# Kernel tuning notes

Measured on AMD Instinct MI355X. Metric: run time of the kernel, lower is better.

Reference implementation:

```python
import jax, jax.numpy as jnp
import numpy as np

N_NODES = 40000
N_EDGES = 640000
D_IN = 512
D_OUT = 128


def setup_inputs() -> dict:
    key = jax.random.key(0)
    k_x, k_w, k_a, k_v, k_r, k_c = jax.random.split(key, 6)
    # Xavier-uniform bound for Linear(in=512, out=128)
    bound = float(np.sqrt(6.0 / (D_IN + D_OUT)))
    x = jax.random.normal(k_x, (N_NODES, D_IN), dtype=jnp.float32)
    weight = jax.random.uniform(k_w, (D_OUT, D_IN), dtype=jnp.float32,
                                minval=-bound, maxval=bound)
    bias = jnp.zeros((D_OUT,), dtype=jnp.float32)
    # PReLU default init is 0.25 (single shared slope)
    alpha = jnp.full((1,), 0.25, dtype=jnp.float32)
    edge_val = jax.random.uniform(k_v, (N_EDGES,), dtype=jnp.float32)
    edge_row = jax.random.randint(k_r, (N_EDGES,), 0, N_NODES, dtype=jnp.int32)
    edge_col = jax.random.randint(k_c, (N_EDGES,), 0, N_NODES, dtype=jnp.int32)
    return {"x": x, "weight": weight, "bias": bias, "alpha": alpha,
            "edge_val": edge_val, "edge_row": edge_row, "edge_col": edge_col}


def reference(x, weight, bias, alpha, edge_val, edge_row, edge_col):
    # seq = fc_1(input): [N, D_out]
    seq = jnp.einsum('ni,oi->no', x, weight)
    # torch.spmm(adj, seq) with adj in COO form:
    # out[r] = sum over edges (r, c, v) of v * seq[c]
    msgs = edge_val[:, None] * seq[edge_col]          # [E, D_out]
    agg = jax.ops.segment_sum(msgs, edge_row, num_segments=x.shape[0])
    agg = agg + bias
    # PReLU with a single shared slope alpha
    return jnp.where(agg > 0, agg, alpha[0] * agg)
```

## Files before the change

kernel.cpp:

```cpp
#include <hip/hip_runtime.h>
#include <hip/hip_bf16.h>

#define N_NODES 40000
#define N_EDGES 640000
#define D_IN 512
#define D_OUT 128
#define BM 128
#define BK 64
#define CAP 128

typedef __attribute__((ext_vector_type(4))) float f32x4;
typedef __attribute__((ext_vector_type(8))) short bf16x8;
typedef __attribute__((ext_vector_type(4))) unsigned short us4;

static __device__ __forceinline__ unsigned short f2bf(float f) {
    unsigned int u = __float_as_uint(f);
    unsigned int r = u + 0x7fffu + ((u >> 16) & 1u);
    return (unsigned short)(r >> 16);
}

__global__ __launch_bounds__(256) void gemm_kernel(
    const float* __restrict__ x, const float* __restrict__ w,
    unsigned short* __restrict__ seq)
{
    __shared__ unsigned short As[BM * BK];
    __shared__ unsigned short Bs[D_OUT * BK];

    const int tid = threadIdx.x;
    const int lane = tid & 63;
    const int wv = tid >> 6;
    const int block_row = blockIdx.x * BM;
    const int srow = tid >> 3;
    const int scol = (tid & 7) * 8;

    f32x4 ra[4][2], rb[4][2];

    auto issue_loads = [&](int k0) {
        #pragma unroll
        for (int p = 0; p < 4; ++p) {
            int gr = block_row + srow + p * 32; if (gr >= N_NODES) gr = N_NODES - 1;
            const float* sa = x + (size_t)gr * D_IN + k0 + scol;
            ra[p][0] = *(const f32x4*)sa;
            ra[p][1] = *(const f32x4*)(sa + 4);
            const float* sb = w + (size_t)(srow + p * 32) * D_IN + k0 + scol;
            rb[p][0] = *(const f32x4*)sb;
            rb[p][1] = *(const f32x4*)(sb + 4);
        }
    };

    f32x4 acc[2][8];
    #pragma unroll
    for (int i = 0; i < 2; i++)
        #pragma unroll
        for (int j = 0; j < 8; j++)
            acc[i][j] = f32x4{0.f, 0.f, 0.f, 0.f};

    issue_loads(0);

    for (int kt = 0; kt < D_IN / BK; ++kt) {
        __syncthreads();
        #pragma unroll
        for (int p = 0; p < 4; ++p) {
            int r = srow + p * 32;
            us4 h0, h1, g0, g1;
            #pragma unroll
            for (int q = 0; q < 4; q++) {
                h0[q] = f2bf(ra[p][0][q]); h1[q] = f2bf(ra[p][1][q]);
                g0[q] = f2bf(rb[p][0][q]); g1[q] = f2bf(rb[p][1][q]);
            }
            int off = (r * (BK * 2) + scol * 2) ^ ((r & 7) << 4);
            *(us4*)((char*)As + off)     = h0;
            *(us4*)((char*)As + off + 8) = h1;
            *(us4*)((char*)Bs + off)     = g0;
            *(us4*)((char*)Bs + off + 8) = g1;
        }
        if (kt < D_IN / BK - 1) issue_loads((kt + 1) * BK);
        __syncthreads();

        #pragma unroll
        for (int ks = 0; ks < 2; ++ks) {
            const int kb = ks * 32 + (lane >> 4) * 8;
            bf16x8 a[2], b[8];
            #pragma unroll
            for (int m = 0; m < 2; m++) {
                int r = wv * 32 + m * 16 + (lane & 15);
                int off = (r * (BK * 2) + kb * 2) ^ ((r & 7) << 4);
                a[m] = *(const bf16x8*)((const char*)As + off);
            }
            #pragma unroll
            for (int n = 0; n < 8; n++) {
                int r = n * 16 + (lane & 15);
                int off = (r * (BK * 2) + kb * 2) ^ ((r & 7) << 4);
                b[n] = *(const bf16x8*)((const char*)Bs + off);
            }
            #pragma unroll
            for (int m = 0; m < 2; m++)
                #pragma unroll
                for (int n = 0; n < 8; n++)
                    acc[m][n] = __builtin_amdgcn_mfma_f32_16x16x32_bf16(a[m], b[n], acc[m][n], 0, 0, 0);
        }
    }

    #pragma unroll
    for (int m = 0; m < 2; m++) {
        #pragma unroll
        for (int r = 0; r < 4; r++) {
            int grow = block_row + wv * 32 + m * 16 + (lane >> 4) * 4 + r;
            if (grow < N_NODES) {
                #pragma unroll
                for (int n = 0; n < 8; n++) {
                    int col = n * 16 + (lane & 15);
                    seq[(size_t)grow * D_OUT + col] = f2bf(acc[m][n][r]);
                }
            }
        }
    }
}

__global__ void zero_kernel(int* __restrict__ p, int n) {
    int i = blockIdx.x * blockDim.x + threadIdx.x;
    if (i < n) p[i] = 0;
}

__global__ void scatter_kernel(
    const int* __restrict__ erow, const int* __restrict__ ecol,
    const float* __restrict__ eval, int* __restrict__ cursor,
    float2* __restrict__ bucket)
{
    int e = blockIdx.x * blockDim.x + threadIdx.x;
    if (e >= N_EDGES) return;
    int r = erow[e];
    int slot = atomicAdd(&cursor[r], 1);
    bucket[(size_t)r * CAP + slot] = make_float2(eval[e], __int_as_float(ecol[e]));
}

__global__ __launch_bounds__(256) void agg_kernel(
    const unsigned short* __restrict__ seq, const int* __restrict__ cursor,
    const float2* __restrict__ bucket, const float* __restrict__ bias,
    const float* __restrict__ alpha, float* __restrict__ out)
{
    const int row = blockIdx.x * 4 + (threadIdx.x >> 6);
    const int lane = threadIdx.x & 63;
    const int cnt = cursor[row];
    const float2* b = bucket + (size_t)row * CAP;

    float a0 = 0.f, a1 = 0.f;
    int e = 0;
    for (; e + 4 <= cnt; e += 4) {
        float2 q0 = b[e], q1 = b[e + 1], q2 = b[e + 2], q3 = b[e + 3];
        unsigned int p0 = *(const unsigned int*)(seq + (size_t)__float_as_uint(q0.y) * D_OUT + lane * 2);
        unsigned int p1 = *(const unsigned int*)(seq + (size_t)__float_as_uint(q1.y) * D_OUT + lane * 2);
        unsigned int p2 = *(const unsigned int*)(seq + (size_t)__float_as_uint(q2.y) * D_OUT + lane * 2);
        unsigned int p3 = *(const unsigned int*)(seq + (size_t)__float_as_uint(q3.y) * D_OUT + lane * 2);
        a0 += q0.x * __uint_as_float(p0 << 16);
        a1 += q0.x * __uint_as_float(p0 & 0xffff0000u);
        a0 += q1.x * __uint_as_float(p1 << 16);
        a1 += q1.x * __uint_as_float(p1 & 0xffff0000u);
        a0 += q2.x * __uint_as_float(p2 << 16);
        a1 += q2.x * __uint_as_float(p2 & 0xffff0000u);
        a0 += q3.x * __uint_as_float(p3 << 16);
        a1 += q3.x * __uint_as_float(p3 & 0xffff0000u);
    }
    for (; e < cnt; ++e) {
        float2 q0 = b[e];
        unsigned int p0 = *(const unsigned int*)(seq + (size_t)__float_as_uint(q0.y) * D_OUT + lane * 2);
        a0 += q0.x * __uint_as_float(p0 << 16);
        a1 += q0.x * __uint_as_float(p0 & 0xffff0000u);
    }
    float al = alpha[0];
    float2 bi = *(const float2*)(bias + lane * 2);
    float r0 = a0 + bi.x;
    float r1 = a1 + bi.y;
    r0 = r0 > 0.f ? r0 : al * r0;
    r1 = r1 > 0.f ? r1 : al * r1;
    *(float2*)(out + (size_t)row * D_OUT + lane * 2) = make_float2(r0, r1);
}

extern "C" void kernel_launch(void* const* d_in, const int* in_sizes, int n_in,
                              void* d_out, int out_size, void* d_ws, size_t ws_size,
                              hipStream_t stream)
{
    (void)in_sizes; (void)n_in; (void)out_size; (void)ws_size;
    const float* x     = (const float*)d_in[0];
    const float* w     = (const float*)d_in[1];
    const float* bias  = (const float*)d_in[2];
    const float* alpha = (const float*)d_in[3];
    const float* eval  = (const float*)d_in[4];
    const int*   erow  = (const int*)d_in[5];
    const int*   ecol  = (const int*)d_in[6];
    float* out = (float*)d_out;

    char* ws = (char*)d_ws;
    unsigned short* seq = (unsigned short*)ws;
    int*    cursor = (int*)(ws + 10240000);
    float2* bucket = (float2*)(ws + 10400000);

    zero_kernel<<<(N_NODES + 255) / 256, 256, 0, stream>>>(cursor, N_NODES);
    scatter_kernel<<<(N_EDGES + 255) / 256, 256, 0, stream>>>(erow, ecol, eval, cursor, bucket);
    gemm_kernel<<<(N_NODES + BM - 1) / BM, 256, 0, stream>>>(x, w, seq);
    agg_kernel<<<N_NODES / 4, 256, 0, stream>>>(seq, cursor, bucket, bias, alpha, out);
}
```

Before: 224.4 us.

## Merge edge scatter into GEMM launch as extra blocks to overlap them

The edge bucketing scatter moves into the GEMM launch as additional blocks, so the memory-bound scatter runs alongside the compute-bound GEMM and one launch disappears. Each scatter thread now handles 4 edges, issuing its loads and atomics together to raise memory-level parallelism. The scatter blocks carry the GEMM's shared memory allocation and register footprint, which may limit how many of them fit per CU. Block order also means the GEMM blocks are dispatched first.

```diff
diff --git a/kernel.cpp b/kernel.cpp
--- a/kernel.cpp
+++ b/kernel.cpp
@@ -8,6 +8,9 @@
 #define BM 128
 #define BK 64
 #define CAP 128
+#define NB_GE 313
+#define EPT 4
+#define NB_SC 625
 
 typedef __attribute__((ext_vector_type(4))) float f32x4;
 typedef __attribute__((ext_vector_type(8))) short bf16x8;
@@ -19,10 +22,36 @@
     return (unsigned short)(r >> 16);
 }
 
-__global__ __launch_bounds__(256) void gemm_kernel(
+__global__ void zero_kernel(int* __restrict__ p, int n) {
+    int i = blockIdx.x * blockDim.x + threadIdx.x;
+    if (i < n) p[i] = 0;
+}
+
+__global__ __launch_bounds__(256) void fused_kernel(
     const float* __restrict__ x, const float* __restrict__ w,
-    unsigned short* __restrict__ seq)
+    unsigned short* __restrict__ seq,
+    const int* __restrict__ erow, const int* __restrict__ ecol,
+    const float* __restrict__ eval, int* __restrict__ cursor,
+    float2* __restrict__ bucket)
 {
+    if (blockIdx.x >= NB_GE) {
+        const int base = (blockIdx.x - NB_GE) * (256 * EPT) + threadIdx.x;
+        int r[EPT], c[EPT];
+        float v[EPT];
+        #pragma unroll
+        for (int k = 0; k < EPT; k++) {
+            int e = base + k * 256;
+            r[k] = erow[e]; c[k] = ecol[e]; v[k] = eval[e];
+        }
+        int slot[EPT];
+        #pragma unroll
+        for (int k = 0; k < EPT; k++) slot[k] = atomicAdd(&cursor[r[k]], 1);
+        #pragma unroll
+        for (int k = 0; k < EPT; k++)
+            bucket[(size_t)r[k] * CAP + slot[k]] = make_float2(v[k], __int_as_float(c[k]));
+        return;
+    }
+
     __shared__ unsigned short As[BM * BK];
     __shared__ unsigned short Bs[D_OUT * BK];
 
@@ -115,23 +144,6 @@
             }
         }
     }
-}
-
-__global__ void zero_kernel(int* __restrict__ p, int n) {
-    int i = blockIdx.x * blockDim.x + threadIdx.x;
-    if (i < n) p[i] = 0;
-}
-
-__global__ void scatter_kernel(
-    const int* __restrict__ erow, const int* __restrict__ ecol,
-    const float* __restrict__ eval, int* __restrict__ cursor,
-    float2* __restrict__ bucket)
-{
-    int e = blockIdx.x * blockDim.x + threadIdx.x;
-    if (e >= N_EDGES) return;
-    int r = erow[e];
-    int slot = atomicAdd(&cursor[r], 1);
-    bucket[(size_t)r * CAP + slot] = make_float2(eval[e], __int_as_float(ecol[e]));
 }
 
 __global__ __launch_bounds__(256) void agg_kernel(
@@ -196,7 +208,6 @@
     float2* bucket = (float2*)(ws + 10400000);
 
     zero_kernel<<<(N_NODES + 255) / 256, 256, 0, stream>>>(cursor, N_NODES);
-    scatter_kernel<<<(N_EDGES + 255) / 256, 256, 0, stream>>>(erow, ecol, eval, cursor, bucket);
-    gemm_kernel<<<(N_NODES + BM - 1) / BM, 256, 0, stream>>>(x, w, seq);
+    fused_kernel<<<NB_GE + NB_SC, 256, 0, stream>>>(x, w, seq, erow, ecol, eval, cursor, bucket);
     agg_kernel<<<N_NODES / 4, 256, 0, stream>>>(seq, cursor, bucket, bias, alpha, out);
 }
```

Measured after the change: 194.2 us. 13.5% less time.
